# Performance work log

Measured on AMD Instinct MI355X. Metric: run time of the kernel, lower is better.

Reference implementation:

```python
import jax, jax.numpy as jnp
import numpy as np

EPS = 1e-5  # GroupNorm eps


def setup_inputs() -> dict:
    key = jax.random.key(0)
    ks = jax.random.split(key, 12)
    D, H, I = 512, 8, 64
    B, L = 2, 1024
    g = 0.01  # xavier gain used in reset_parameters
    inp = {
        "x": jax.random.normal(ks[0], (B, L, D), jnp.float32),
        "w_z": jax.random.normal(ks[1], (D, D), jnp.float32) * g,
        "b_z": jnp.zeros((D,), jnp.float32),
        "w_za": jax.random.normal(ks[2], (D, D), jnp.float32) * g,
        "b_za": jnp.zeros((D,), jnp.float32),
        "w_ang": jax.random.normal(ks[3], (D, H), jnp.float32) * g,
        "b_ang": jnp.zeros((H,), jnp.float32),
        "w_abs": jax.random.normal(ks[4], (D, H), jnp.float32) * g,
        "b_abs": jnp.zeros((H,), jnp.float32),
        "w_y": jax.random.normal(ks[5], (D, D), jnp.float32) * g,
        "b_y": jnp.zeros((D,), jnp.float32),
        "w_ya": jax.random.normal(ks[6], (D, D), jnp.float32) * g,
        "b_ya": jnp.zeros((D,), jnp.float32),
        "gn_w": jnp.ones((H,), jnp.float32),
        "gn_b": jnp.zeros((H,), jnp.float32),
        "lc_r": jax.random.normal(ks[7], (H, I), jnp.float32),
        "lc_i": jax.random.normal(ks[8], (H, I), jnp.float32),
    }
    return inp


def reference(x, w_z, b_z, w_za, b_za, w_ang, b_ang, w_abs, b_abs,
              w_y, b_y, w_ya, b_ya, gn_w, gn_b, lc_r, lc_i):
    B, L, D = x.shape
    H = gn_w.shape[0]
    I = D // H
    silu = jax.nn.silu
    xf = x.astype(jnp.float32)

    # gated value, promoted to complex:  [B, L, H, I]
    z = ((xf @ w_z + b_z) * silu(xf @ w_za + b_za)).astype(jnp.complex64).reshape(B, L, H, I)

    # per-head log-decay phazor: [B, L, H] complex
    scale = (0.001 ** jnp.linspace(0.0, 1.0, H)).astype(jnp.float32)
    ln_ph = (silu(xf @ w_ang + b_ang) * 1j - jax.nn.sigmoid(xf @ w_abs + b_abs)) * scale

    # FFT of ones => circular conv with ones = cumulative sum along axis 1
    ones_fft = jnp.fft.fft(jnp.ones((L,), jnp.float32), n=2 * L)

    # ln_phazor repeated over m then tril(-1) over the LAST TWO dims (m, h),
    # exactly matching torch.Tensor.tril semantics on a 'b l m h' tensor.
    masked = jnp.tril(jnp.broadcast_to(ln_ph[:, :, None, :], (B, L, L, H)), -1)
    mfft = jnp.fft.fft(masked, n=2 * L, axis=1)
    mconv = jnp.fft.ifft(mfft * ones_fft[None, :, None, None], axis=1)[:, :L]
    ph_masked = jnp.tril(jnp.exp(mconv))  # tril over (m, h)

    h_inner = jnp.einsum('blmh,bmhi->blhi', ph_masked, z)

    pfft = jnp.fft.fft(ln_ph, n=2 * L, axis=1)
    pconv = jnp.fft.ifft(pfft * ones_fft[None, :, None], axis=1)[:, :L]
    last_conv = lc_r + 1j * lc_i  # [H, I] complex (last_conv_init broadcast over batch)
    h_cross = jnp.exp(pconv)[..., None] * last_conv[None, None]  # [B, L, H, I]

    h = (h_inner + h_cross).real  # [B, L, H, I]

    # GroupNorm(H groups, H channels) on (B*L, H, I): per-(sample, head) norm over I
    mean = h.mean(axis=-1, keepdims=True)
    var = h.var(axis=-1, keepdims=True)
    hn = (h - mean) / jnp.sqrt(var + EPS) * gn_w[:, None] + gn_b[:, None]
    h_norm = hn.reshape(B, L, D)

    y = (h_norm @ w_y + b_y) * silu(xf @ w_ya + b_ya)
    return y.astype(x.dtype)
```

## Files before the change

kernel.cpp:

```cpp
#include <hip/hip_runtime.h>
#include <math.h>

#define D_ 512
#define H_ 8
#define I_ 64
#define L_ 1024

typedef __attribute__((ext_vector_type(8))) short short8;
typedef __attribute__((ext_vector_type(4))) float f32x4;

__device__ __forceinline__ float sigmoidf_(float x) { return 1.f / (1.f + expf(-x)); }
__device__ __forceinline__ float siluf_(float x) { return x / (1.f + expf(-x)); }

__device__ __forceinline__ unsigned short f2bf(float f) {
    unsigned u = __float_as_uint(f);
    u += 0x7fffu + ((u >> 16) & 1u);
    return (unsigned short)(u >> 16);
}
__device__ __forceinline__ float bf2f(unsigned short v) {
    return __uint_as_float((unsigned)v << 16);
}

#define RS 80
#define RSS 40

__global__ __launch_bounds__(256) void k1_prep(
    const float* __restrict__ x,
    const float* __restrict__ w0, const float* __restrict__ w1,
    const float* __restrict__ w2, const float* __restrict__ w3,
    unsigned short* __restrict__ t0, unsigned short* __restrict__ t1,
    unsigned short* __restrict__ t2, unsigned short* __restrict__ t3,
    const float* __restrict__ w_ang, const float* __restrict__ b_ang,
    const float* __restrict__ w_abs, const float* __restrict__ b_abs,
    float* __restrict__ a_out, float* __restrict__ r_out)
{
    __shared__ float sm[64][65];
    const int tid = threadIdx.x;
    const int bid = blockIdx.x;
    if (bid < 256) {
        int zsel = bid >> 6, tile = bid & 63;
        const float* src = zsel == 0 ? w0 : zsel == 1 ? w1 : zsel == 2 ? w2 : w3;
        unsigned short* dst = zsel == 0 ? t0 : zsel == 1 ? t1 : zsel == 2 ? t2 : t3;
        const int k0 = (tile >> 3) * 64, n0 = (tile & 7) * 64;
#pragma unroll
        for (int i = 0; i < 16; ++i) {
            int idx = tid + i * 256;
            int rr = idx >> 6, cc = idx & 63;
            sm[rr][cc] = src[(size_t)(k0 + rr) * 512 + n0 + cc];
        }
        __syncthreads();
#pragma unroll
        for (int i = 0; i < 16; ++i) {
            int idx = tid + i * 256;
            int rr = idx >> 6, cc = idx & 63;
            dst[(size_t)(n0 + rr) * 512 + k0 + cc] = f2bf(sm[cc][rr]);
        }
        return;
    }
    {
        int t = bid - 256;
        const int s = tid & 3, c = (tid >> 2) & 15, r = tid >> 6;
        const int n = t * 4 + r;
        const int h = c & 7;
        const float* wp = (c < 8) ? w_ang : w_abs;
        const float* xr = x + (size_t)n * D_;
        float acc = 0.f;
#pragma unroll 4
        for (int i = 0; i < 128; ++i) {
            int k = i * 4 + s;
            acc = fmaf(xr[k], wp[k * H_ + h], acc);
        }
        acc += __shfl_xor(acc, 1);
        acc += __shfl_xor(acc, 2);
        if (s == 0) {
            const float scale = expf(-6.9077552789821368f * (h * (1.0f / 7.0f)));
            if (c < 8) { float p = acc + b_ang[h]; a_out[(size_t)n * H_ + h] = siluf_(p) * scale; }
            else       { float p = acc + b_abs[h]; r_out[(size_t)n * H_ + h] = sigmoidf_(p) * scale; }
        }
    }
}

__global__ __launch_bounds__(256) void k2_split(
    const float* __restrict__ x,
    const unsigned short* __restrict__ Wz, const unsigned short* __restrict__ Wza,
    const unsigned short* __restrict__ Wya,
    const float* __restrict__ b_z, const float* __restrict__ b_za, const float* __restrict__ b_ya,
    unsigned short* __restrict__ gateb, float* __restrict__ Zs_part, float* __restrict__ zdiag,
    const float* __restrict__ a_arr, const float* __restrict__ r_arr,
    float* __restrict__ Si, float* __restrict__ Sr)
{
    __shared__ short As[2][64 * RSS];
    __shared__ short Bs[2][2][64 * RSS];
    __shared__ float red[64][8];
    __shared__ float2 buf[2][256];
    const int tid = threadIdx.x;
    const int bid = blockIdx.x;

    if (bid < 16) {
        const int b = bid >> 3, h = bid & 7;
        float2 v[4];
        float2 run = make_float2(0.f, 0.f);
        const size_t base = ((size_t)b * L_ + tid * 4) * H_ + h;
#pragma unroll
        for (int j = 0; j < 4; ++j) {
            run.x += a_arr[base + j * H_];
            run.y += r_arr[base + j * H_];
            v[j] = run;
        }
        buf[0][tid] = run;
        __syncthreads();
        int src = 0;
        for (int off = 1; off < 256; off <<= 1) {
            float2 val = buf[src][tid];
            if (tid >= off) { float2 q = buf[src][tid - off]; val.x += q.x; val.y += q.y; }
            buf[src ^ 1][tid] = val;
            src ^= 1;
            __syncthreads();
        }
        float2 excl = make_float2(0.f, 0.f);
        if (tid > 0) excl = buf[src][tid - 1];
#pragma unroll
        for (int j = 0; j < 4; ++j) {
            Si[base + j * H_] = v[j].x + excl.x;
            Sr[base + j * H_] = -(v[j].y + excl.y);
        }
        return;
    }

    const bool zza = bid < 272;
    const int u = zza ? (bid - 16) : (bid - 272);
    const int rblk = (u & 7) * 4 + (u >> 6);
    const int bx = (u >> 3) & 7;
    const int lane = tid & 63, w = tid >> 6;
    const int wm = w >> 1, wn = w & 1;
    const int row0 = rblk * 64, col0 = bx * 64;

    const f32x4 zf = {0.f, 0.f, 0.f, 0.f};
    const int sr_ = tid >> 2, sc_ = tid & 3;
    const int sld = sr_ * RS + sc_ * 16;
    const float* gAx = x + (size_t)(row0 + sr_) * 512 + sc_ * 8;
    const int ck = (lane >> 4) << 4;

    if (zza) {
        const unsigned short* gWz  = Wz  + (size_t)(col0 + sr_) * 512 + sc_ * 8;
        const unsigned short* gWza = Wza + (size_t)(col0 + sr_) * 512 + sc_ * 8;
        f32x4 accz[2][2], accza[2][2];
#pragma unroll
        for (int a = 0; a < 2; ++a)
#pragma unroll
            for (int bq = 0; bq < 2; ++bq) { accz[a][bq] = zf; accza[a][bq] = zf; }

        float4 ra0, ra1; int4 rz, rza;
#define Z_LOAD(K) { ra0 = *(const float4*)(gAx + (K)); ra1 = *(const float4*)(gAx + (K) + 4); \
                    rz  = *(const int4*)(gWz  + (K)); rza = *(const int4*)(gWza + (K)); }
#define Z_WRITE(BUF) { short8 ab; \
                       ab[0]=(short)f2bf(ra0.x); ab[1]=(short)f2bf(ra0.y); \
                       ab[2]=(short)f2bf(ra0.z); ab[3]=(short)f2bf(ra0.w); \
                       ab[4]=(short)f2bf(ra1.x); ab[5]=(short)f2bf(ra1.y); \
                       ab[6]=(short)f2bf(ra1.z); ab[7]=(short)f2bf(ra1.w); \
                       *(short8*)((char*)As[BUF] + sld) = ab; \
                       *(int4*)((char*)Bs[BUF][0] + sld) = rz; \
                       *(int4*)((char*)Bs[BUF][1] + sld) = rza; }

        Z_LOAD(0);
        Z_WRITE(0);
        Z_LOAD(32);
        __syncthreads();

        int cur = 0;
        for (int s = 0; s < 16; ++s) {
            if (s < 15) {
                Z_WRITE(cur ^ 1);
                if (s < 14) Z_LOAD((s + 2) * 32);
            }
            short8 af[2], bz[2], bza[2];
#pragma unroll
            for (int fi = 0; fi < 2; ++fi) {
                int rr = wm * 32 + fi * 16 + (lane & 15);
                af[fi] = *(const short8*)((const char*)As[cur] + rr * RS + ck);
            }
#pragma unroll
            for (int fj = 0; fj < 2; ++fj) {
                int rr = wn * 32 + fj * 16 + (lane & 15);
                bz[fj]  = *(const short8*)((const char*)Bs[cur][0] + rr * RS + ck);
                bza[fj] = *(const short8*)((const char*)Bs[cur][1] + rr * RS + ck);
            }
#pragma unroll
            for (int fi = 0; fi < 2; ++fi)
#pragma unroll
                for (int fj = 0; fj < 2; ++fj) {
                    accz[fi][fj]  = __builtin_amdgcn_mfma_f32_16x16x32_bf16(af[fi], bz[fj],  accz[fi][fj],  0, 0, 0);
                    accza[fi][fj] = __builtin_amdgcn_mfma_f32_16x16x32_bf16(af[fi], bza[fj], accza[fi][fj], 0, 0, 0);
                }
            __syncthreads();
            cur ^= 1;
        }
#undef Z_LOAD
#undef Z_WRITE

        const bool first = (rblk & 15) == 0;
        const int b8 = (rblk >> 4) * 8;
#pragma unroll
        for (int fj = 0; fj < 2; ++fj) {
            float lsum = 0.f;
            int lc = wn * 32 + fj * 16 + (lane & 15);
            int col = col0 + lc;
            float Bz = b_z[col], Bza = b_za[col];
#pragma unroll
            for (int fi = 0; fi < 2; ++fi) {
#pragma unroll
                for (int q = 0; q < 4; ++q) {
                    int lr = wm * 32 + fi * 16 + ((lane >> 4) << 2) + q;
                    float pz = accz[fi][fj][q] + Bz;
                    float pza = accza[fi][fj][q] + Bza;
                    float v = pz * siluf_(pza);
                    if (!first || lr > bx) lsum += v;
                    if (first && lr == bx) zdiag[(b8 + bx) * 64 + lc] = v;
                }
            }
            red[lc][wm * 4 + (lane >> 4)] = lsum;
        }
        __syncthreads();
        if (tid < 64) {
            float s = 0.f;
#pragma unroll
            for (int j = 0; j < 8; ++j) s += red[tid][j];
            Zs_part[((size_t)rblk * 8 + bx) * 64 + tid] = s;
        }
    } else {
        const unsigned short* gWya = Wya + (size_t)(col0 + sr_) * 512 + sc_ * 8;
        f32x4 accya[2][2];
#pragma unroll
        for (int a = 0; a < 2; ++a)
#pragma unroll
            for (int bq = 0; bq < 2; ++bq) accya[a][bq] = zf;

        float4 ra0, ra1; int4 rya;
#define Y_LOAD(K) { ra0 = *(const float4*)(gAx + (K)); ra1 = *(const float4*)(gAx + (K) + 4); \
                    rya = *(const int4*)(gWya + (K)); }
#define Y_WRITE(BUF) { short8 ab; \
                       ab[0]=(short)f2bf(ra0.x); ab[1]=(short)f2bf(ra0.y); \
                       ab[2]=(short)f2bf(ra0.z); ab[3]=(short)f2bf(ra0.w); \
                       ab[4]=(short)f2bf(ra1.x); ab[5]=(short)f2bf(ra1.y); \
                       ab[6]=(short)f2bf(ra1.z); ab[7]=(short)f2bf(ra1.w); \
                       *(short8*)((char*)As[BUF] + sld) = ab; \
                       *(int4*)((char*)Bs[BUF][0] + sld) = rya; }

        Y_LOAD(0);
        Y_WRITE(0);
        Y_LOAD(32);
        __syncthreads();

        int cur = 0;
        for (int s = 0; s < 16; ++s) {
            if (s < 15) {
                Y_WRITE(cur ^ 1);
                if (s < 14) Y_LOAD((s + 2) * 32);
            }
            short8 af[2], bya[2];
#pragma unroll
            for (int fi = 0; fi < 2; ++fi) {
                int rr = wm * 32 + fi * 16 + (lane & 15);
                af[fi] = *(const short8*)((const char*)As[cur] + rr * RS + ck);
            }
#pragma unroll
            for (int fj = 0; fj < 2; ++fj) {
                int rr = wn * 32 + fj * 16 + (lane & 15);
                bya[fj] = *(const short8*)((const char*)Bs[cur][0] + rr * RS + ck);
            }
#pragma unroll
            for (int fi = 0; fi < 2; ++fi)
#pragma unroll
                for (int fj = 0; fj < 2; ++fj)
                    accya[fi][fj] = __builtin_amdgcn_mfma_f32_16x16x32_bf16(af[fi], bya[fj], accya[fi][fj], 0, 0, 0);
            __syncthreads();
            cur ^= 1;
        }
#undef Y_LOAD
#undef Y_WRITE

#pragma unroll
        for (int fj = 0; fj < 2; ++fj) {
            int lc = wn * 32 + fj * 16 + (lane & 15);
            int col = col0 + lc;
            float Bya = b_ya[col];
#pragma unroll
            for (int fi = 0; fi < 2; ++fi)
#pragma unroll
                for (int q = 0; q < 4; ++q) {
                    int lr = wm * 32 + fi * 16 + ((lane >> 4) << 2) + q;
                    int row = row0 + lr;
                    gateb[(size_t)row * 512 + col] = f2bf(siluf_(accya[fi][fj][q] + Bya));
                }
        }
    }
}

__global__ __launch_bounds__(512) void k3_hgn_gemm_y(
    const unsigned short* __restrict__ Wy, const float* __restrict__ b_y,
    const unsigned short* __restrict__ gateb,
    const float* __restrict__ Sr, const float* __restrict__ Si,
    const float* __restrict__ Zs_part, const float* __restrict__ zdiag,
    const float* __restrict__ lc_r, const float* __restrict__ lc_i,
    const float* __restrict__ gn_w, const float* __restrict__ gn_b,
    float* __restrict__ y)
{
    __shared__ unsigned short hA[64][520];
    __shared__ short Bs[2][64 * RSS];
    __shared__ float Cr[8][65], Ci[8][65], Zd[8][65];
    const int tid = threadIdx.x;
    const int lane = tid & 63, w = tid >> 6;
    const int cbx = blockIdx.x & 7;
    const int rpair = blockIdx.x >> 3;
    const int row0 = rpair * 64, col0 = cbx * 64;
    const int b = row0 >> 10;

    const int brow = tid >> 3, bsc = tid & 7;
    const size_t gB = (size_t)(col0 + brow) * 512 + bsc * 4;
    const int bwr = brow * RS + bsc * 8;
    int2 rw0 = *(const int2*)(Wy + gB);
    int2 rw1 = *(const int2*)(Wy + gB + 32);

    {
        int h = tid >> 6, i = tid & 63;
        float s = 0.f;
#pragma unroll
        for (int rb = 0; rb < 16; ++rb)
            s += Zs_part[(((size_t)b * 16 + rb) * 8 + h) * 64 + i];
        Cr[h][i] = s + lc_r[h * 64 + i];
        Ci[h][i] = lc_i[h * 64 + i];
        Zd[h][i] = zdiag[((size_t)b * 8 + h) * 64 + i];
    }
    __syncthreads();

    {
        const int r = tid >> 3, h = tid & 7;
        const int row = row0 + r;
        const float sr = Sr[(size_t)row * 8 + h];
        const float si = Si[(size_t)row * 8 + h];
        const float er = expf(sr);
        const float ca = er * cosf(si), sb = er * sinf(si);
        float sum = 0.f, sq = 0.f;
#pragma unroll 8
        for (int i = 0; i < 64; ++i) {
            float hv = Zd[h][i] + ca * Cr[h][i] - sb * Ci[h][i];
            sum += hv; sq += hv * hv;
        }
        const float mean = sum * (1.f / 64.f);
        const float inv = rsqrtf(sq * (1.f / 64.f) - mean * mean + 1e-5f);
        const float gw = gn_w[h] * inv;
        const float gb = gn_b[h] - mean * gw;
#pragma unroll
        for (int s8 = 0; s8 < 8; ++s8) {
            short8 pk;
#pragma unroll
            for (int j = 0; j < 8; ++j) {
                int i = s8 * 8 + j;
                float hv = Zd[h][i] + ca * Cr[h][i] - sb * Ci[h][i];
                pk[j] = (short)f2bf(hv * gw + gb);
            }
            int slot = (s8 + h) & 7;
            *(short8*)((char*)&hA[r][0] + h * 128 + slot * 16) = pk;
        }
    }
    *(int2*)((char*)Bs[0] + bwr) = rw0;
    __syncthreads();

    const int wm = w >> 2, wn = w & 3;
    const f32x4 zf = {0.f, 0.f, 0.f, 0.f};
    f32x4 acc[2] = {zf, zf};

    int cur = 0;
    for (int s = 0; s < 16; ++s) {
        if (s < 15) {
            *(int2*)((char*)Bs[cur ^ 1] + bwr) = rw1;
            if (s < 14) rw1 = *(const int2*)(Wy + gB + (s + 2) * 32);
        }
        const int k0 = s * 32;
        short8 af[2], bf;
        const int hk = k0 >> 6;
        const int t = ((k0 & 32) >> 3) + (lane >> 4);
        const int slot = (t + hk) & 7;
#pragma unroll
        for (int fi = 0; fi < 2; ++fi) {
            int rr = wm * 32 + fi * 16 + (lane & 15);
            af[fi] = *(const short8*)((const char*)&hA[rr][0] + hk * 128 + slot * 16);
        }
        {
            int rr = wn * 16 + (lane & 15);
            bf = *(const short8*)((const char*)Bs[cur] + rr * RS + ((lane >> 4) << 4));
        }
        acc[0] = __builtin_amdgcn_mfma_f32_16x16x32_bf16(af[0], bf, acc[0], 0, 0, 0);
        acc[1] = __builtin_amdgcn_mfma_f32_16x16x32_bf16(af[1], bf, acc[1], 0, 0, 0);
        __syncthreads();
        cur ^= 1;
    }

    const int col = col0 + wn * 16 + (lane & 15);
    const float By = b_y[col];
#pragma unroll
    for (int fi = 0; fi < 2; ++fi)
#pragma unroll
        for (int q = 0; q < 4; ++q) {
            int row = row0 + wm * 32 + fi * 16 + ((lane >> 4) << 2) + q;
            size_t idx = (size_t)row * 512 + col;
            y[idx] = (acc[fi][q] + By) * bf2f(gateb[idx]);
        }
}

extern "C" void kernel_launch(void* const* d_in, const int* in_sizes, int n_in,
                              void* d_out, int out_size, void* d_ws, size_t ws_size,
                              hipStream_t stream) {
    (void)n_in; (void)out_size; (void)ws_size;
    const float* x     = (const float*)d_in[0];
    const float* w_z   = (const float*)d_in[1];
    const float* b_z   = (const float*)d_in[2];
    const float* w_za  = (const float*)d_in[3];
    const float* b_za  = (const float*)d_in[4];
    const float* w_ang = (const float*)d_in[5];
    const float* b_ang = (const float*)d_in[6];
    const float* w_abs = (const float*)d_in[7];
    const float* b_abs = (const float*)d_in[8];
    const float* w_y   = (const float*)d_in[9];
    const float* b_y   = (const float*)d_in[10];
    const float* w_ya  = (const float*)d_in[11];
    const float* b_ya  = (const float*)d_in[12];
    const float* gn_w  = (const float*)d_in[13];
    const float* gn_b  = (const float*)d_in[14];
    const float* lc_r  = (const float*)d_in[15];
    const float* lc_i  = (const float*)d_in[16];
    float* y = (float*)d_out;

    const int BL = in_sizes[0] / D_;
    const int B  = BL / L_;

    unsigned short* wtz  = (unsigned short*)d_ws;
    unsigned short* wtza = wtz  + 512 * 512;
    unsigned short* wtya = wtza + 512 * 512;
    unsigned short* wty  = wtya + 512 * 512;
    unsigned short* gateb= wty  + 512 * 512;
    float* a_arr = (float*)(gateb + (size_t)BL * 512);
    float* r_arr = a_arr + (size_t)BL * H_;
    float* Si    = r_arr + (size_t)BL * H_;
    float* Sr    = Si    + (size_t)BL * H_;
    float* zdiag = Sr    + (size_t)BL * H_;
    float* Zs_part = zdiag + (size_t)B * H_ * I_;

    const int ntiles = (BL / 64) * 8;

    k1_prep<<<256 + BL / 4, 256, 0, stream>>>(
        x, w_z, w_za, w_ya, w_y, wtz, wtza, wtya, wty,
        w_ang, b_ang, w_abs, b_abs, a_arr, r_arr);
    k2_split<<<16 + 2 * ntiles, 256, 0, stream>>>(
        x, wtz, wtza, wtya, b_z, b_za, b_ya,
        gateb, Zs_part, zdiag, a_arr, r_arr, Si, Sr);
    k3_hgn_gemm_y<<<ntiles, 512, 0, stream>>>(
        wty, b_y, gateb, Sr, Si, Zs_part, zdiag, lc_r, lc_i, gn_w, gn_b, y);
}
```

Measured before the change: 40.48 us.

## Pre-convert x to bf16 once in prep kernel and halve k3 row tiles

The prep kernel now stages each group of 4 x rows in shared memory and writes a bf16 copy of x to workspace. The GEMM kernel reads that copy directly, so it no longer loads fp32 x and converts it per tile. This halves x read traffic in k2 and removes repeated conversion work across column tiles. Separately, k3 now uses 32-row tiles with 256 threads, launching twice as many blocks with less shared memory each for better occupancy, at the cost of recomputing the per-block Zs/GroupNorm prologue more times.

```diff
diff --git a/kernel.cpp b/kernel.cpp
--- a/kernel.cpp
+++ b/kernel.cpp
@@ -25,7 +25,7 @@
 #define RSS 40
 
 __global__ __launch_bounds__(256) void k1_prep(
-    const float* __restrict__ x,
+    const float* __restrict__ x, unsigned short* __restrict__ xb,
     const float* __restrict__ w0, const float* __restrict__ w1,
     const float* __restrict__ w2, const float* __restrict__ w3,
     unsigned short* __restrict__ t0, unsigned short* __restrict__ t1,
@@ -58,12 +58,23 @@
         return;
     }
     {
-        int t = bid - 256;
+        float* xs = &sm[0][0];
+        const int t = bid - 256;
+        const int n0 = t * 4;
+#pragma unroll
+        for (int p = 0; p < 2; ++p) {
+            int idx = (p * 256 + tid) * 4;
+            int rr = idx >> 9, cc = idx & 511;
+            float4 v = *(const float4*)(x + (size_t)(n0 + rr) * 512 + cc);
+            *(float4*)(xs + idx) = v;
+            ushort4 o = { f2bf(v.x), f2bf(v.y), f2bf(v.z), f2bf(v.w) };
+            *(ushort4*)(xb + (size_t)(n0 + rr) * 512 + cc) = o;
+        }
+        __syncthreads();
         const int s = tid & 3, c = (tid >> 2) & 15, r = tid >> 6;
-        const int n = t * 4 + r;
         const int h = c & 7;
         const float* wp = (c < 8) ? w_ang : w_abs;
-        const float* xr = x + (size_t)n * D_;
+        const float* xr = xs + r * 512;
         float acc = 0.f;
 #pragma unroll 4
         for (int i = 0; i < 128; ++i) {
@@ -73,6 +84,7 @@
         acc += __shfl_xor(acc, 1);
         acc += __shfl_xor(acc, 2);
         if (s == 0) {
+            const int n = n0 + r;
             const float scale = expf(-6.9077552789821368f * (h * (1.0f / 7.0f)));
             if (c < 8) { float p = acc + b_ang[h]; a_out[(size_t)n * H_ + h] = siluf_(p) * scale; }
             else       { float p = acc + b_abs[h]; r_out[(size_t)n * H_ + h] = sigmoidf_(p) * scale; }
@@ -81,7 +93,7 @@
 }
 
 __global__ __launch_bounds__(256) void k2_split(
-    const float* __restrict__ x,
+    const unsigned short* __restrict__ xb,
     const unsigned short* __restrict__ Wz, const unsigned short* __restrict__ Wza,
     const unsigned short* __restrict__ Wya,
     const float* __restrict__ b_z, const float* __restrict__ b_za, const float* __restrict__ b_ya,
@@ -138,7 +150,7 @@
     const f32x4 zf = {0.f, 0.f, 0.f, 0.f};
     const int sr_ = tid >> 2, sc_ = tid & 3;
     const int sld = sr_ * RS + sc_ * 16;
-    const float* gAx = x + (size_t)(row0 + sr_) * 512 + sc_ * 8;
+    const unsigned short* gXa = xb + (size_t)(row0 + sr_) * 512 + sc_ * 8;
     const int ck = (lane >> 4) << 4;
 
     if (zza) {
@@ -150,15 +162,10 @@
 #pragma unroll
             for (int bq = 0; bq < 2; ++bq) { accz[a][bq] = zf; accza[a][bq] = zf; }
 
-        float4 ra0, ra1; int4 rz, rza;
-#define Z_LOAD(K) { ra0 = *(const float4*)(gAx + (K)); ra1 = *(const float4*)(gAx + (K) + 4); \
+        int4 rxa, rz, rza;
+#define Z_LOAD(K) { rxa = *(const int4*)(gXa + (K)); \
                     rz  = *(const int4*)(gWz  + (K)); rza = *(const int4*)(gWza + (K)); }
-#define Z_WRITE(BUF) { short8 ab; \
-                       ab[0]=(short)f2bf(ra0.x); ab[1]=(short)f2bf(ra0.y); \
-                       ab[2]=(short)f2bf(ra0.z); ab[3]=(short)f2bf(ra0.w); \
-                       ab[4]=(short)f2bf(ra1.x); ab[5]=(short)f2bf(ra1.y); \
-                       ab[6]=(short)f2bf(ra1.z); ab[7]=(short)f2bf(ra1.w); \
-                       *(short8*)((char*)As[BUF] + sld) = ab; \
+#define Z_WRITE(BUF) { *(int4*)((char*)As[BUF] + sld) = rxa; \
                        *(int4*)((char*)Bs[BUF][0] + sld) = rz; \
                        *(int4*)((char*)Bs[BUF][1] + sld) = rza; }
 
@@ -235,15 +242,9 @@
 #pragma unroll
             for (int bq = 0; bq < 2; ++bq) accya[a][bq] = zf;
 
-        float4 ra0, ra1; int4 rya;
-#define Y_LOAD(K) { ra0 = *(const float4*)(gAx + (K)); ra1 = *(const float4*)(gAx + (K) + 4); \
-                    rya = *(const int4*)(gWya + (K)); }
-#define Y_WRITE(BUF) { short8 ab; \
-                       ab[0]=(short)f2bf(ra0.x); ab[1]=(short)f2bf(ra0.y); \
-                       ab[2]=(short)f2bf(ra0.z); ab[3]=(short)f2bf(ra0.w); \
-                       ab[4]=(short)f2bf(ra1.x); ab[5]=(short)f2bf(ra1.y); \
-                       ab[6]=(short)f2bf(ra1.z); ab[7]=(short)f2bf(ra1.w); \
-                       *(short8*)((char*)As[BUF] + sld) = ab; \
+        int4 rxa, rya;
+#define Y_LOAD(K) { rxa = *(const int4*)(gXa + (K)); rya = *(const int4*)(gWya + (K)); }
+#define Y_WRITE(BUF) { *(int4*)((char*)As[BUF] + sld) = rxa; \
                        *(int4*)((char*)Bs[BUF][0] + sld) = rya; }
 
         Y_LOAD(0);
@@ -296,7 +297,7 @@
     }
 }
 
-__global__ __launch_bounds__(512) void k3_hgn_gemm_y(
+__global__ __launch_bounds__(256) void k3_hgn_gemm_y(
     const unsigned short* __restrict__ Wy, const float* __restrict__ b_y,
     const unsigned short* __restrict__ gateb,
     const float* __restrict__ Sr, const float* __restrict__ Si,
@@ -305,24 +306,24 @@
     const float* __restrict__ gn_w, const float* __restrict__ gn_b,
     float* __restrict__ y)
 {
-    __shared__ unsigned short hA[64][520];
+    __shared__ unsigned short hA[32][520];
     __shared__ short Bs[2][64 * RSS];
     __shared__ float Cr[8][65], Ci[8][65], Zd[8][65];
     const int tid = threadIdx.x;
     const int lane = tid & 63, w = tid >> 6;
     const int cbx = blockIdx.x & 7;
-    const int rpair = blockIdx.x >> 3;
-    const int row0 = rpair * 64, col0 = cbx * 64;
+    const int rsub = blockIdx.x >> 3;
+    const int row0 = rsub * 32, col0 = cbx * 64;
     const int b = row0 >> 10;
 
-    const int brow = tid >> 3, bsc = tid & 7;
-    const size_t gB = (size_t)(col0 + brow) * 512 + bsc * 4;
-    const int bwr = brow * RS + bsc * 8;
-    int2 rw0 = *(const int2*)(Wy + gB);
-    int2 rw1 = *(const int2*)(Wy + gB + 32);
-
-    {
-        int h = tid >> 6, i = tid & 63;
+    const int brow = tid >> 2, bsc = tid & 3;
+    const size_t gB = (size_t)(col0 + brow) * 512 + bsc * 8;
+    const int bwr = brow * RS + bsc * 16;
+    int4 rw0 = *(const int4*)(Wy + gB);
+    int4 rw1 = *(const int4*)(Wy + gB + 32);
+
+    for (int uu = tid; uu < 512; uu += 256) {
+        int h = uu >> 6, i = uu & 63;
         float s = 0.f;
 #pragma unroll
         for (int rb = 0; rb < 16; ++rb)
@@ -363,18 +364,17 @@
             *(short8*)((char*)&hA[r][0] + h * 128 + slot * 16) = pk;
         }
     }
-    *(int2*)((char*)Bs[0] + bwr) = rw0;
+    *(int4*)((char*)Bs[0] + bwr) = rw0;
     __syncthreads();
 
-    const int wm = w >> 2, wn = w & 3;
     const f32x4 zf = {0.f, 0.f, 0.f, 0.f};
     f32x4 acc[2] = {zf, zf};
 
     int cur = 0;
     for (int s = 0; s < 16; ++s) {
         if (s < 15) {
-            *(int2*)((char*)Bs[cur ^ 1] + bwr) = rw1;
-            if (s < 14) rw1 = *(const int2*)(Wy + gB + (s + 2) * 32);
+            *(int4*)((char*)Bs[cur ^ 1] + bwr) = rw1;
+            if (s < 14) rw1 = *(const int4*)(Wy + gB + (s + 2) * 32);
         }
         const int k0 = s * 32;
         short8 af[2], bf;
@@ -383,11 +383,11 @@
         const int slot = (t + hk) & 7;
 #pragma unroll
         for (int fi = 0; fi < 2; ++fi) {
-            int rr = wm * 32 + fi * 16 + (lane & 15);
+            int rr = fi * 16 + (lane & 15);
             af[fi] = *(const short8*)((const char*)&hA[rr][0] + hk * 128 + slot * 16);
         }
         {
-            int rr = wn * 16 + (lane & 15);
+            int rr = w * 16 + (lane & 15);
             bf = *(const short8*)((const char*)Bs[cur] + rr * RS + ((lane >> 4) << 4));
         }
         acc[0] = __builtin_amdgcn_mfma_f32_16x16x32_bf16(af[0], bf, acc[0], 0, 0, 0);
@@ -396,13 +396,13 @@
         cur ^= 1;
     }
 
-    const int col = col0 + wn * 16 + (lane & 15);
+    const int col = col0 + w * 16 + (lane & 15);
     const float By = b_y[col];
 #pragma unroll
     for (int fi = 0; fi < 2; ++fi)
 #pragma unroll
         for (int q = 0; q < 4; ++q) {
-            int row = row0 + wm * 32 + fi * 16 + ((lane >> 4) << 2) + q;
+            int row = row0 + fi * 16 + ((lane >> 4) << 2) + q;
             size_t idx = (size_t)row * 512 + col;
             y[idx] = (acc[fi][q] + By) * bf2f(gateb[idx]);
         }
@@ -439,7 +439,8 @@
     unsigned short* wtya = wtza + 512 * 512;
     unsigned short* wty  = wtya + 512 * 512;
     unsigned short* gateb= wty  + 512 * 512;
-    float* a_arr = (float*)(gateb + (size_t)BL * 512);
+    unsigned short* xb   = gateb + (size_t)BL * 512;
+    float* a_arr = (float*)(xb + (size_t)BL * 512);
     float* r_arr = a_arr + (size_t)BL * H_;
     float* Si    = r_arr + (size_t)BL * H_;
     float* Sr    = Si    + (size_t)BL * H_;
@@ -449,11 +450,11 @@
     const int ntiles = (BL / 64) * 8;
 
     k1_prep<<<256 + BL / 4, 256, 0, stream>>>(
-        x, w_z, w_za, w_ya, w_y, wtz, wtza, wtya, wty,
+        x, xb, w_z, w_za, w_ya, w_y, wtz, wtza, wtya, wty,
         w_ang, b_ang, w_abs, b_abs, a_arr, r_arr);
     k2_split<<<16 + 2 * ntiles, 256, 0, stream>>>(
-        x, wtz, wtza, wtya, b_z, b_za, b_ya,
+        xb, wtz, wtza, wtya, b_z, b_za, b_ya,
         gateb, Zs_part, zdiag, a_arr, r_arr, Si, Sr);
-    k3_hgn_gemm_y<<<ntiles, 512, 0, stream>>>(
+    k3_hgn_gemm_y<<<2 * ntiles, 256, 0, stream>>>(
         wty, b_y, gateb, Sr, Si, Zs_part, zdiag, lc_r, lc_i, gn_w, gn_b, y);
 }
```

After: 40.40 us (median of 3 runs). Within noise of the previous version (-0.2%).
